# Kernel optimization log

Hardware: AMD Instinct MI355X
Metric: run time of the kernel (lower is better)

Reference implementation:

```python
import jax, jax.numpy as jnp
import numpy as np
import math

B, T, D = 4, 2048, 1024
NHEAD = 16
HEAD_DIM = D // NHEAD
MAX_REL = 16  # max_relative_position default


def setup_inputs() -> dict:
    key = jax.random.key(0)
    ks = jax.random.split(key, 10)
    s = 1.0 / math.sqrt(D)
    inp = {
        "x": jax.random.normal(ks[0], (B, T, D), dtype=jnp.float32),
        "Wq": jax.random.normal(ks[1], (D, D), dtype=jnp.float32) * s,
        "bq": jnp.zeros((D,), dtype=jnp.float32),
        "Wk": jax.random.normal(ks[2], (D, D), dtype=jnp.float32) * s,
        "bk": jnp.zeros((D,), dtype=jnp.float32),
        "Wv": jax.random.normal(ks[3], (D, D), dtype=jnp.float32) * s,
        "bv": jnp.zeros((D,), dtype=jnp.float32),
        "rel_bias": jax.random.normal(ks[4], (2 * MAX_REL - 1, NHEAD), dtype=jnp.float32) * 0.02,
        "Wo": jax.random.normal(ks[5], (D, D), dtype=jnp.float32) * s,
        "bo": jnp.zeros((D,), dtype=jnp.float32),
    }
    return inp


def _relative_bias(rel_bias, seq_len):
    # distance matrix clamped to [-(MAX_REL-1), MAX_REL-1], shifted to index table
    r = jnp.arange(seq_len)
    dist = jnp.clip(r[None, :] - r[:, None], -MAX_REL + 1, MAX_REL - 1) + MAX_REL - 1
    # gather: [T, T, H] -> [H, T, T]
    return jnp.transpose(rel_bias[dist], (2, 0, 1))


def reference(x, Wq, bq, Wk, bk, Wv, bv, rel_bias, Wo, bo):
    Bdim, Tdim, Ddim = x.shape
    # torch Linear: x @ W.T + b
    Q = x @ Wq.T + bq
    K = x @ Wk.T + bk
    V = x @ Wv.T + bv
    # [B, H, T, hd]
    Q = Q.reshape(Bdim, Tdim, NHEAD, HEAD_DIM).transpose(0, 2, 1, 3)
    K = K.reshape(Bdim, Tdim, NHEAD, HEAD_DIM).transpose(0, 2, 1, 3)
    V = V.reshape(Bdim, Tdim, NHEAD, HEAD_DIM).transpose(0, 2, 1, 3)
    scores = jnp.einsum("bhqd,bhkd->bhqk", Q, K) / math.sqrt(HEAD_DIM)
    scores = scores + _relative_bias(rel_bias, Tdim)[None]  # [1,H,T,T]
    attn = jax.nn.softmax(scores, axis=-1)
    out = jnp.einsum("bhqk,bhkd->bhqd", attn, V)
    out = out.transpose(0, 2, 1, 3).reshape(Bdim, Tdim, Ddim)
    return out @ Wo.T + bo
```

## Files before the change

kernel.cpp:

```cpp
#include <hip/hip_runtime.h>
#include <stdint.h>
#include <math.h>

typedef unsigned short u16;
typedef __bf16 bf16x8 __attribute__((ext_vector_type(8)));
typedef float f32x4 __attribute__((ext_vector_type(4)));
typedef float f32x2 __attribute__((ext_vector_type(2)));
typedef float f32x16 __attribute__((ext_vector_type(16)));
typedef unsigned short u16x8 __attribute__((ext_vector_type(8)));
typedef unsigned short u16x4 __attribute__((ext_vector_type(4)));

#define BATCH 4
#define SEQT 2048
#define DMODEL 1024
#define NHEAD 16
#define HDIM 64
#define LOG2E 1.44269504f

#define LDS_GLD16(gp, lp)                                                     \
  __builtin_amdgcn_global_load_lds(                                           \
      (const __attribute__((address_space(1))) void*)(gp),                    \
      (__attribute__((address_space(3))) void*)(lp), 16, 0, 0)

static __device__ __forceinline__ u16 f2bf(float f) {
  union { float f; uint32_t u; } c; c.f = f;
  uint32_t u = c.u;
  return (u16)((u + 0x7fffu + ((u >> 16) & 1u)) >> 16);
}
static __device__ __forceinline__ u16 f2bf_fast(float f) {
  union { float f; uint32_t u; } c; c.f = f;
  return (u16)((c.u + 0x8000u) >> 16);
}
static __device__ __forceinline__ uint32_t pkbf(float a, float b) {
  union { float f; uint32_t u; } ca, cb; ca.f = a; cb.f = b;
  return __builtin_amdgcn_perm(cb.u + 0x8000u, ca.u + 0x8000u, 0x07060302u);
}
static __device__ __forceinline__ bf16x8 mk_bf8(uint32_t x0, uint32_t x1,
                                                uint32_t x2, uint32_t x3) {
  union { uint32_t u[4]; bf16x8 v; } t;
  t.u[0] = x0; t.u[1] = x1; t.u[2] = x2; t.u[3] = x3;
  return t.v;
}

__global__ __launch_bounds__(256) void k_convert_all(
    const float* __restrict__ x, const float* __restrict__ Wq,
    const float* __restrict__ Wk, const float* __restrict__ Wv,
    const float* __restrict__ Wo, u16* __restrict__ xbf,
    u16* __restrict__ Wqkv, u16* __restrict__ Wob) {
  const int NX4 = 2097152, NW4 = 262144;
  int i = blockIdx.x * 256 + threadIdx.x;
  const float* s; u16* d; int js, jd;
  if (i < NX4) {
    s = x; d = xbf; js = jd = i;
  } else if (i < NX4 + 3 * NW4) {
    int j = i - NX4;
    int w = j >> 18;
    s = (w == 0) ? Wq : (w == 1) ? Wk : Wv;
    js = j & (NW4 - 1);
    d = Wqkv; jd = j;
  } else {
    s = Wo; d = Wob; js = jd = i - NX4 - 3 * NW4;
  }
  float4 v = ((const float4*)s)[js];
  u16x4 o = {f2bf(v.x), f2bf(v.y), f2bf(v.z), f2bf(v.w)};
  ((u16x4*)d)[jd] = o;
}

__global__ __launch_bounds__(256) void k_gemm_qkvt(
    const u16* __restrict__ xbf, const u16* __restrict__ Wqk,
    const u16* __restrict__ Wv, const float* __restrict__ bq_,
    const float* __restrict__ bk_, const float* __restrict__ bv_,
    u16* __restrict__ dq, u16* __restrict__ dk, u16* __restrict__ Vt) {
  __shared__ u16 As[128 * 64];
  __shared__ u16 Bs[128 * 64];

  const int bid = blockIdx.x;
  const bool isQK = bid < 1024;
  const u16 *Ap, *Bp;
  int m0, n0;
  if (isQK) {
    m0 = (bid & 63) * 128; n0 = (bid >> 6) * 128; Ap = xbf; Bp = Wqk;
  } else {
    int j = bid - 1024;
    m0 = (j & 7) * 128; n0 = (j >> 3) * 128; Ap = Wv; Bp = xbf;
  }

  const int tid = threadIdx.x;
  const int wave = tid >> 6, lane = tid & 63;
  const int quad = lane >> 4, l16 = lane & 15;
  const int wm = wave & 1, wn = wave >> 1;
  const int lrow = lane >> 3, lcol = (lane & 7) * 8;

  f32x4 acc[4][4] = {};

  for (int kt = 0; kt < 1024; kt += 64) {
    __syncthreads();
    for (int c = 0; c < 4; ++c) {
      int rr = (wave * 4 + c) * 8 + lrow;
      LDS_GLD16(Ap + (size_t)(m0 + rr) * 1024 + kt + lcol,
                &As[(wave * 4 + c) * 512]);
      LDS_GLD16(Bp + (size_t)(n0 + rr) * 1024 + kt + lcol,
                &Bs[(wave * 4 + c) * 512]);
    }
    __syncthreads();
    for (int kh = 0; kh < 2; ++kh) {
      bf16x8 af[4], bfr[4];
      for (int mt = 0; mt < 4; ++mt)
        af[mt] = *(const bf16x8*)&As[(wm * 64 + mt * 16 + l16) * 64 + kh * 32 +
                                     quad * 8];
      for (int nt = 0; nt < 4; ++nt)
        bfr[nt] = *(const bf16x8*)&Bs[(wn * 64 + nt * 16 + l16) * 64 + kh * 32 +
                                      quad * 8];
      for (int mt = 0; mt < 4; ++mt)
        for (int nt = 0; nt < 4; ++nt)
          acc[mt][nt] = __builtin_amdgcn_mfma_f32_16x16x32_bf16(
              af[mt], bfr[nt], acc[mt][nt], 0, 0, 0);
    }
  }

  if (isQK) {
    u16* dst = (n0 < 1024) ? dq : dk;
    const float* bias = (n0 < 1024) ? bq_ : bk_;
    for (int mt = 0; mt < 4; ++mt)
      for (int nt = 0; nt < 4; ++nt) {
        int nn = (n0 + wn * 64 + nt * 16 + l16) & 1023;
        float bv = bias[nn];
        int h = nn >> 6, hd = nn & 63;
        for (int r = 0; r < 4; ++r) {
          int m = m0 + wm * 64 + mt * 16 + quad * 4 + r;
          int b = m >> 11, t = m & 2047;
          dst[(((size_t)b * NHEAD + h) * SEQT + t) * HDIM + hd] =
              f2bf_fast(acc[mt][nt][r] + bv);
        }
      }
  } else {
    for (int mt = 0; mt < 4; ++mt)
      for (int nt = 0; nt < 4; ++nt) {
        int n = n0 + wn * 64 + nt * 16 + l16;
        int b = n >> 11, t = n & 2047;
        int tp = (t & ~15) | ((t & 4) << 1) | ((t & 8) >> 1) | (t & 3);
        for (int r = 0; r < 4; ++r) {
          int m = m0 + wm * 64 + mt * 16 + quad * 4 + r;
          float v = acc[mt][nt][r] + bv_[m];
          Vt[((size_t)(b * NHEAD + (m >> 6)) * HDIM + (m & 63)) * SEQT + tp] =
              f2bf_fast(v);
        }
      }
  }
}

__global__ __launch_bounds__(256) void k_gemm_proj(const u16* __restrict__ A,
                                                   const u16* __restrict__ Bm,
                                                   const float* __restrict__ bias,
                                                   float* __restrict__ out) {
  __shared__ u16 As[128 * 64];
  __shared__ u16 Bs[128 * 64];

  const int tid = threadIdx.x;
  const int wave = tid >> 6, lane = tid & 63;
  const int quad = lane >> 4, l16 = lane & 15;
  const int wm = wave & 1, wn = wave >> 1;
  const int m0 = blockIdx.x * 128, n0 = blockIdx.y * 128;
  const int lrow = lane >> 3, lcol = (lane & 7) * 8;

  f32x4 acc[4][4] = {};

  for (int kt = 0; kt < 1024; kt += 64) {
    __syncthreads();
    for (int c = 0; c < 4; ++c) {
      int rr = (wave * 4 + c) * 8 + lrow;
      LDS_GLD16(A + (size_t)(m0 + rr) * 1024 + kt + lcol,
                &As[(wave * 4 + c) * 512]);
      LDS_GLD16(Bm + (size_t)(n0 + rr) * 1024 + kt + lcol,
                &Bs[(wave * 4 + c) * 512]);
    }
    __syncthreads();
    for (int kh = 0; kh < 2; ++kh) {
      bf16x8 af[4], bfr[4];
      for (int mt = 0; mt < 4; ++mt)
        af[mt] = *(const bf16x8*)&As[(wm * 64 + mt * 16 + l16) * 64 + kh * 32 +
                                     quad * 8];
      for (int nt = 0; nt < 4; ++nt)
        bfr[nt] = *(const bf16x8*)&Bs[(wn * 64 + nt * 16 + l16) * 64 + kh * 32 +
                                      quad * 8];
      for (int mt = 0; mt < 4; ++mt)
        for (int nt = 0; nt < 4; ++nt)
          acc[mt][nt] = __builtin_amdgcn_mfma_f32_16x16x32_bf16(
              af[mt], bfr[nt], acc[mt][nt], 0, 0, 0);
    }
  }

  for (int mt = 0; mt < 4; ++mt)
    for (int nt = 0; nt < 4; ++nt) {
      int n = n0 + wn * 64 + nt * 16 + l16;
      float bv = bias[n];
      for (int r = 0; r < 4; ++r) {
        int m = m0 + wm * 64 + mt * 16 + quad * 4 + r;
        out[(size_t)m * 1024 + n] = acc[mt][nt][r] + bv;
      }
    }
}

__global__ __launch_bounds__(256)
__attribute__((amdgpu_waves_per_eu(4, 4)))
void k_attn(const u16* __restrict__ Qb, const u16* __restrict__ Kb,
            const u16* __restrict__ Vt, const float* __restrict__ relb,
            u16* __restrict__ Obf) {
  __shared__ u16 Ks[64 * 64];
  __shared__ u16 VTs[64 * 64];
  __shared__ float biasL[32];

  const int tid = threadIdx.x;
  const int wave = tid >> 6, lane = tid & 63;
  const int l32 = lane & 31, hi = lane >> 5;
  const int qt = blockIdx.x;
  const int bh = blockIdx.y;
  const int h = bh & (NHEAD - 1);
  const size_t base = (size_t)bh * SEQT * HDIM;
  const int qa = qt * 128 + wave * 32;

  if (tid < 31) biasL[tid] = relb[tid * NHEAD + h] * LOG2E;
  const float bLo = relb[0 * NHEAD + h] * LOG2E;
  const float bHi = relb[30 * NHEAD + h] * LOG2E;
  const float CL = 0.125f * LOG2E;

  bf16x8 bq[4];
  {
    const u16* qp = Qb + base + (size_t)(qa + l32) * HDIM + hi * 8;
    for (int ds = 0; ds < 4; ++ds) bq[ds] = *(const bf16x8*)(qp + ds * 16);
  }

  f32x16 Oacc[2] = {};
  f32x2 ls2 = {};

  const int rl = lane >> 3, gb = lane & 7;
  const int row0 = wave * 8 + rl, row1 = row0 + 32;
  const u16* kgp0 = Kb + base + (size_t)row0 * HDIM + ((gb ^ (row0 & 7)) << 3);
  const u16* kgp1 = Kb + base + (size_t)row1 * HDIM + ((gb ^ (row1 & 7)) << 3);
  const u16* vgp0 = Vt + base + (size_t)row0 * SEQT + ((gb ^ (row0 & 7)) << 3);
  const u16* vgp1 = Vt + base + (size_t)row1 * SEQT + ((gb ^ (row1 & 7)) << 3);
  u16* ksl0 = &Ks[wave * 512 + lane * 8];
  u16* ksl1 = ksl0 + 2048;
  u16* vsl0 = &VTs[wave * 512 + lane * 8];
  u16* vsl1 = vsl0 + 2048;

  int akoff[8], avoff[8];
#pragma unroll
  for (int kgrp = 0; kgrp < 2; ++kgrp) {
    const int key = kgrp * 32 + l32;
#pragma unroll
    for (int ds = 0; ds < 4; ++ds)
      akoff[kgrp * 4 + ds] = key * 64 + (((ds * 2 + hi) ^ (key & 7)) << 3);
#pragma unroll
    for (int ks = 0; ks < 2; ++ks)
#pragma unroll
      for (int dg = 0; dg < 2; ++dg) {
        const int d = dg * 32 + l32;
        const int blk = kgrp * 4 + ks * 2 + hi;
        avoff[(kgrp * 2 + ks) * 2 + dg] = d * 64 + ((blk ^ (d & 7)) << 3);
      }
  }

  for (int kt2 = 0; kt2 < 32; ++kt2) {
    const int k0 = kt2 * 64;
    __syncthreads();
    LDS_GLD16(kgp0 + (size_t)k0 * HDIM, ksl0);
    LDS_GLD16(kgp1 + (size_t)k0 * HDIM, ksl1);
    LDS_GLD16(vgp0 + k0, vsl0);
    LDS_GLD16(vgp1 + k0, vsl1);
    __syncthreads();

#pragma unroll
    for (int kgrp = 0; kgrp < 2; ++kgrp) {
      const int kb = k0 + kgrp * 32;
      f32x16 c = {};
#pragma unroll
      for (int ds = 0; ds < 4; ++ds) {
        bf16x8 ak = *(const bf16x8*)&Ks[akoff[kgrp * 4 + ds]];
        c = __builtin_amdgcn_mfma_f32_32x32x16_bf16(ak, bq[ds], c, 0, 0, 0);
      }

      const int dmin = kb - (qa + 31);
      if (dmin >= 15 || kb + 31 - qa <= -15) {
        const float ub = (dmin >= 15) ? bHi : bLo;
#pragma unroll
        for (int i = 0; i < 16; ++i)
          c[i] = __builtin_amdgcn_exp2f(fmaf(c[i], CL, ub));
      } else {
        const int dbase = kb + 4 * hi - (qa + l32);
#pragma unroll
        for (int i = 0; i < 16; ++i) {
          int d = dbase + (i & 3) + 8 * (i >> 2);
          d = d < -15 ? -15 : (d > 15 ? 15 : d);
          c[i] = __builtin_amdgcn_exp2f(fmaf(c[i], CL, biasL[d + 15]));
        }
      }
      {
        f32x2 s0 = {c[0], c[1]}, s1 = {c[2], c[3]};
        f32x2 s2 = {c[4], c[5]}, s3 = {c[6], c[7]};
        f32x2 s4 = {c[8], c[9]}, s5 = {c[10], c[11]};
        f32x2 s6 = {c[12], c[13]}, s7 = {c[14], c[15]};
        ls2 += ((s0 + s1) + (s2 + s3)) + ((s4 + s5) + (s6 + s7));
      }

      uint32_t p[8];
#pragma unroll
      for (int i = 0; i < 8; ++i) p[i] = pkbf(c[2 * i], c[2 * i + 1]);

#pragma unroll
      for (int ks = 0; ks < 2; ++ks) {
        bf16x8 bp = mk_bf8(p[ks * 4 + 0], p[ks * 4 + 1], p[ks * 4 + 2],
                           p[ks * 4 + 3]);
#pragma unroll
        for (int dg = 0; dg < 2; ++dg) {
          bf16x8 av = *(const bf16x8*)&VTs[avoff[(kgrp * 2 + ks) * 2 + dg]];
          Oacc[dg] = __builtin_amdgcn_mfma_f32_32x32x16_bf16(av, bp, Oacc[dg],
                                                             0, 0, 0);
        }
      }
    }
  }

  float ls = ls2.x + ls2.y;
  ls += __shfl_xor(ls, 32, 64);
  const float rinv = 1.0f / ls;

  const int b = bh >> 4;
  const int t = qa + l32;
  u16* op = Obf + ((size_t)(b * SEQT + t)) * DMODEL + h * HDIM;
#pragma unroll
  for (int dg = 0; dg < 2; ++dg)
#pragma unroll
    for (int a = 0; a < 4; ++a) {
      uint2 w;
      w.x = pkbf(Oacc[dg][4 * a + 0] * rinv, Oacc[dg][4 * a + 1] * rinv);
      w.y = pkbf(Oacc[dg][4 * a + 2] * rinv, Oacc[dg][4 * a + 3] * rinv);
      *(uint2*)(op + dg * 32 + 8 * a + 4 * hi) = w;
    }
}

extern "C" void kernel_launch(void* const* d_in, const int* in_sizes, int n_in,
                              void* d_out, int out_size, void* d_ws,
                              size_t ws_size, hipStream_t stream) {
  const float* x = (const float*)d_in[0];
  const float* Wq = (const float*)d_in[1];
  const float* bq = (const float*)d_in[2];
  const float* Wk = (const float*)d_in[3];
  const float* bk = (const float*)d_in[4];
  const float* Wv = (const float*)d_in[5];
  const float* bv = (const float*)d_in[6];
  const float* relb = (const float*)d_in[7];
  const float* Wo = (const float*)d_in[8];
  const float* bo = (const float*)d_in[9];
  float* out = (float*)d_out;

  char* ws = (char*)d_ws;
  const size_t SZ_X = (size_t)BATCH * SEQT * DMODEL * 2;
  const size_t SZ_W = (size_t)DMODEL * DMODEL * 2;
  u16* xbf = (u16*)(ws);
  u16* Wqb = (u16*)(ws + SZ_X);
  u16* Wvb = (u16*)(ws + SZ_X + 2 * SZ_W);
  u16* Wob = (u16*)(ws + SZ_X + 3 * SZ_W);
  u16* Qb = (u16*)(ws + SZ_X + 4 * SZ_W);
  u16* Kb = (u16*)(ws + 2 * SZ_X + 4 * SZ_W);
  u16* Vt = (u16*)(ws + 3 * SZ_X + 4 * SZ_W);
  u16* Obf = (u16*)(ws + 4 * SZ_X + 4 * SZ_W);

  k_convert_all<<<12288, 256, 0, stream>>>(x, Wq, Wk, Wv, Wo, xbf, Wqb, Wob);
  k_gemm_qkvt<<<1536, 256, 0, stream>>>(xbf, Wqb, Wvb, bq, bk, bv, Qb, Kb, Vt);
  k_attn<<<dim3(16, 64), 256, 0, stream>>>(Qb, Kb, Vt, relb, Obf);
  k_gemm_proj<<<dim3(64, 8), 256, 0, stream>>>(Obf, Wob, bo, out);
}
```

Before: 302.9 us.

## Double-buffer K/V tiles in attention, remap blocks per XCD, use hardware bf16 pack

```diff
diff --git a/kernel.cpp b/kernel.cpp
--- a/kernel.cpp
+++ b/kernel.cpp
@@ -34,6 +34,11 @@
 static __device__ __forceinline__ uint32_t pkbf(float a, float b) {
   union { float f; uint32_t u; } ca, cb; ca.f = a; cb.f = b;
   return __builtin_amdgcn_perm(cb.u + 0x8000u, ca.u + 0x8000u, 0x07060302u);
+}
+static __device__ __forceinline__ uint32_t cvtpk(float a, float b) {
+  uint32_t r;
+  asm("v_cvt_pk_bf16_f32 %0, %1, %2" : "=v"(r) : "v"(a), "v"(b));
+  return r;
 }
 static __device__ __forceinline__ bf16x8 mk_bf8(uint32_t x0, uint32_t x1,
                                                 uint32_t x2, uint32_t x3) {
@@ -201,20 +206,78 @@
     }
 }
 
+#define ATTN_STAGE(NB, KN)                                                    \
+  LDS_GLD16(kgp0 + (size_t)(KN) * HDIM, ksl0 + (NB) * 4096);                  \
+  LDS_GLD16(kgp1 + (size_t)(KN) * HDIM, ksl1 + (NB) * 4096);                  \
+  LDS_GLD16(vgp0 + (KN), vsl0 + (NB) * 4096);                                 \
+  LDS_GLD16(vgp1 + (KN), vsl1 + (NB) * 4096);
+
+#define ATTN_TILE(BUFOFF, K0)                                                 \
+  _Pragma("unroll")                                                           \
+  for (int kgrp = 0; kgrp < 2; ++kgrp) {                                      \
+    const int kb = (K0) + kgrp * 32;                                          \
+    f32x16 c = {};                                                            \
+    _Pragma("unroll")                                                         \
+    for (int ds = 0; ds < 4; ++ds) {                                          \
+      bf16x8 ak = *(const bf16x8*)&Ks[(BUFOFF) + akoff[kgrp * 4 + ds]];       \
+      c = __builtin_amdgcn_mfma_f32_32x32x16_bf16(ak, bq[ds], c, 0, 0, 0);    \
+    }                                                                         \
+    const int dmin = kb - (qa + 31);                                          \
+    if (dmin >= 15 || kb + 31 - qa <= -15) {       \
+      const float ub = (dmin >= 15) ? bHi : bLo;                              \
+      _Pragma("unroll")                                                       \
+      for (int i = 0; i < 16; ++i)                                            \
+        c[i] = __builtin_amdgcn_exp2f(fmaf(c[i], CL, ub));                    \
+    } else {                                                                  \
+      const int dbase = kb + 4 * hi - (qa + l32);                             \
+      _Pragma("unroll")                                                       \
+      for (int i = 0; i < 16; ++i) {                                          \
+        int d = dbase + (i & 3) + 8 * (i >> 2);                               \
+        d = d < -15 ? -15 : (d > 15 ? 15 : d);                                \
+        c[i] = __builtin_amdgcn_exp2f(fmaf(c[i], CL, biasL[d + 15]));         \
+      }                                                                       \
+    }                                                                         \
+    {                                                                         \
+      f32x2 s0 = {c[0], c[1]}, s1 = {c[2], c[3]};                             \
+      f32x2 s2 = {c[4], c[5]}, s3 = {c[6], c[7]};                             \
+      f32x2 s4 = {c[8], c[9]}, s5 = {c[10], c[11]};                           \
+      f32x2 s6 = {c[12], c[13]}, s7 = {c[14], c[15]};                         \
+      ls2 += ((s0 + s1) + (s2 + s3)) + ((s4 + s5) + (s6 + s7));               \
+    }                                                                         \
+    uint32_t p[8];                                                            \
+    _Pragma("unroll")                                                         \
+    for (int i = 0; i < 8; ++i) p[i] = cvtpk(c[2 * i], c[2 * i + 1]);         \
+    _Pragma("unroll")                                                         \
+    for (int ks = 0; ks < 2; ++ks) {                                          \
+      bf16x8 bp = mk_bf8(p[ks * 4 + 0], p[ks * 4 + 1], p[ks * 4 + 2],         \
+                         p[ks * 4 + 3]);                                      \
+      _Pragma("unroll")                                                       \
+      for (int dg = 0; dg < 2; ++dg) {                                        \
+        bf16x8 av = *(const bf16x8*)&VTs[(BUFOFF) +                           \
+                                         avoff[(kgrp * 2 + ks) * 2 + dg]];    \
+        Oacc[dg] = __builtin_amdgcn_mfma_f32_32x32x16_bf16(av, bp, Oacc[dg],  \
+                                                           0, 0, 0);          \
+      }                                                                       \
+    }                                                                         \
+  }
+
 __global__ __launch_bounds__(256)
 __attribute__((amdgpu_waves_per_eu(4, 4)))
 void k_attn(const u16* __restrict__ Qb, const u16* __restrict__ Kb,
             const u16* __restrict__ Vt, const float* __restrict__ relb,
             u16* __restrict__ Obf) {
-  __shared__ u16 Ks[64 * 64];
-  __shared__ u16 VTs[64 * 64];
+  __shared__ u16 Ks[2 * 64 * 64];
+  __shared__ u16 VTs[2 * 64 * 64];
   __shared__ float biasL[32];
 
   const int tid = threadIdx.x;
   const int wave = tid >> 6, lane = tid & 63;
   const int l32 = lane & 31, hi = lane >> 5;
-  const int qt = blockIdx.x;
-  const int bh = blockIdx.y;
+  const int lin = blockIdx.x;
+  const int xcd = lin & 7;
+  const int ixc = lin >> 3;
+  const int bh = xcd * 8 + (ixc & 7);
+  const int qt = ixc >> 3;
   const int h = bh & (NHEAD - 1);
   const size_t base = (size_t)bh * SEQT * HDIM;
   const int qa = qt * 128 + wave * 32;
@@ -261,64 +324,17 @@
       }
   }
 
-  for (int kt2 = 0; kt2 < 32; ++kt2) {
+  ATTN_STAGE(0, 0);
+  __syncthreads();
+
+  for (int kt2 = 0; kt2 < 32; kt2 += 2) {
     const int k0 = kt2 * 64;
-    __syncthreads();
-    LDS_GLD16(kgp0 + (size_t)k0 * HDIM, ksl0);
-    LDS_GLD16(kgp1 + (size_t)k0 * HDIM, ksl1);
-    LDS_GLD16(vgp0 + k0, vsl0);
-    LDS_GLD16(vgp1 + k0, vsl1);
-    __syncthreads();
-
-#pragma unroll
-    for (int kgrp = 0; kgrp < 2; ++kgrp) {
-      const int kb = k0 + kgrp * 32;
-      f32x16 c = {};
-#pragma unroll
-      for (int ds = 0; ds < 4; ++ds) {
-        bf16x8 ak = *(const bf16x8*)&Ks[akoff[kgrp * 4 + ds]];
-        c = __builtin_amdgcn_mfma_f32_32x32x16_bf16(ak, bq[ds], c, 0, 0, 0);
-      }
-
-      const int dmin = kb - (qa + 31);
-      if (dmin >= 15 || kb + 31 - qa <= -15) {
-        const float ub = (dmin >= 15) ? bHi : bLo;
-#pragma unroll
-        for (int i = 0; i < 16; ++i)
-          c[i] = __builtin_amdgcn_exp2f(fmaf(c[i], CL, ub));
-      } else {
-        const int dbase = kb + 4 * hi - (qa + l32);
-#pragma unroll
-        for (int i = 0; i < 16; ++i) {
-          int d = dbase + (i & 3) + 8 * (i >> 2);
-          d = d < -15 ? -15 : (d > 15 ? 15 : d);
-          c[i] = __builtin_amdgcn_exp2f(fmaf(c[i], CL, biasL[d + 15]));
-        }
-      }
-      {
-        f32x2 s0 = {c[0], c[1]}, s1 = {c[2], c[3]};
-        f32x2 s2 = {c[4], c[5]}, s3 = {c[6], c[7]};
-        f32x2 s4 = {c[8], c[9]}, s5 = {c[10], c[11]};
-        f32x2 s6 = {c[12], c[13]}, s7 = {c[14], c[15]};
-        ls2 += ((s0 + s1) + (s2 + s3)) + ((s4 + s5) + (s6 + s7));
-      }
-
-      uint32_t p[8];
-#pragma unroll
-      for (int i = 0; i < 8; ++i) p[i] = pkbf(c[2 * i], c[2 * i + 1]);
-
-#pragma unroll
-      for (int ks = 0; ks < 2; ++ks) {
-        bf16x8 bp = mk_bf8(p[ks * 4 + 0], p[ks * 4 + 1], p[ks * 4 + 2],
-                           p[ks * 4 + 3]);
-#pragma unroll
-        for (int dg = 0; dg < 2; ++dg) {
-          bf16x8 av = *(const bf16x8*)&VTs[avoff[(kgrp * 2 + ks) * 2 + dg]];
-          Oacc[dg] = __builtin_amdgcn_mfma_f32_32x32x16_bf16(av, bp, Oacc[dg],
-                                                             0, 0, 0);
-        }
-      }
-    }
+    ATTN_STAGE(1, k0 + 64);
+    ATTN_TILE(0, k0);
+    __syncthreads();
+    if (kt2 < 30) { ATTN_STAGE(0, k0 + 128); }
+    ATTN_TILE(4096, k0 + 64);
+    __syncthreads();
   }
 
   float ls = ls2.x + ls2.y;
@@ -333,8 +349,8 @@
 #pragma unroll
     for (int a = 0; a < 4; ++a) {
       uint2 w;
-      w.x = pkbf(Oacc[dg][4 * a + 0] * rinv, Oacc[dg][4 * a + 1] * rinv);
-      w.y = pkbf(Oacc[dg][4 * a + 2] * rinv, Oacc[dg][4 * a + 3] * rinv);
+      w.x = cvtpk(Oacc[dg][4 * a + 0] * rinv, Oacc[dg][4 * a + 1] * rinv);
+      w.y = cvtpk(Oacc[dg][4 * a + 2] * rinv, Oacc[dg][4 * a + 3] * rinv);
       *(uint2*)(op + dg * 32 + 8 * a + 4 * hi) = w;
     }
 }
@@ -368,6 +384,6 @@
 
   k_convert_all<<<12288, 256, 0, stream>>>(x, Wq, Wk, Wv, Wo, xbf, Wqb, Wob);
   k_gemm_qkvt<<<1536, 256, 0, stream>>>(xbf, Wqb, Wvb, bq, bk, bv, Qb, Kb, Vt);
-  k_attn<<<dim3(16, 64), 256, 0, stream>>>(Qb, Kb, Vt, relb, Obf);
+  k_attn<<<1024, 256, 0, stream>>>(Qb, Kb, Vt, relb, Obf);
   k_gemm_proj<<<dim3(64, 8), 256, 0, stream>>>(Obf, Wob, bo, out);
 }
```

New measurement: 375.1 us. 1.24x slower.
